# Kernel optimization log

Hardware: AMD Instinct MI355X
Metric: run time of the kernel (lower is better)

Reference implementation:

```python
import jax, jax.numpy as jnp
import numpy as np

EPS = 1e-5

def _conv3x3(x, w, b):
    # standard 3x3 conv, stride 1, padding 1, NCHW/OIHW
    y = jax.lax.conv_general_dilated(x, w, window_strides=(1, 1), padding=((1, 1), (1, 1)),
                                     dimension_numbers=('NCHW', 'OIHW', 'NCHW'))
    return y + b[None, :, None, None]

def _deform_sample(x, offset):
    # x: [B,C,H,W], offset: [B,2*9,H,W] (per kernel point: (dy,dx), torchvision layout)
    # returns bilinear-sampled im2col columns [B,C,9,H,W] with zero padding outside
    B, C, H, W = x.shape
    off = offset.reshape(B, 9, 2, H, W)
    off_y, off_x = off[:, :, 0], off[:, :, 1]                      # [B,9,H,W]
    k = jnp.arange(9)
    ky = (k // 3 - 1).astype(x.dtype)                               # kernel dy in {-1,0,1}
    kx = (k % 3 - 1).astype(x.dtype)                                # kernel dx in {-1,0,1}
    py = jnp.arange(H, dtype=x.dtype)[None, None, :, None] + ky[None, :, None, None] + off_y
    px = jnp.arange(W, dtype=x.dtype)[None, None, None, :] + kx[None, :, None, None] + off_x
    y0 = jnp.floor(py)
    x0 = jnp.floor(px)
    xf = x.reshape(B, C, H * W)
    acc = jnp.zeros((B, C, 9, H, W), x.dtype)
    for dy in (0.0, 1.0):
        for dx in (0.0, 1.0):
            iy = y0 + dy
            ix = x0 + dx
            wgt = (1.0 - jnp.abs(py - iy)) * (1.0 - jnp.abs(px - ix))
            valid = (iy >= 0) & (iy <= H - 1) & (ix >= 0) & (ix <= W - 1)
            wgt = jnp.where(valid, wgt, 0.0)
            idx = jnp.clip(iy, 0, H - 1).astype(jnp.int32) * W + jnp.clip(ix, 0, W - 1).astype(jnp.int32)
            g = jax.vmap(lambda xb, ib: jnp.take(xb, ib, axis=1))(xf, idx.reshape(B, -1))
            acc = acc + wgt[:, None] * g.reshape(B, C, 9, H, W)
    return acc

def setup_inputs() -> dict:
    key = jax.random.key(0)
    ks = jax.random.split(key, 9)
    B, C, O, H, W = 8, 64, 64, 160, 160
    x = jax.random.normal(ks[0], (B, C, H, W), jnp.float32)
    w_off = jax.random.normal(ks[1], (18, C, 3, 3), jnp.float32) * 0.01
    b_off = jax.random.normal(ks[2], (18,), jnp.float32) * 0.01
    w_dcn = jax.random.normal(ks[3], (O, C, 3, 3), jnp.float32) / np.sqrt(C * 9)
    b_dcn = jax.random.normal(ks[4], (O,), jnp.float32) * 0.01
    gamma = 1.0 + 0.1 * jax.random.normal(ks[5], (O,), jnp.float32)
    beta = 0.1 * jax.random.normal(ks[6], (O,), jnp.float32)
    run_mean = 0.1 * jax.random.normal(ks[7], (O,), jnp.float32)
    run_var = 0.5 + jax.random.uniform(ks[8], (O,), jnp.float32)
    return {"x": x, "w_off": w_off, "b_off": b_off, "w_dcn": w_dcn, "b_dcn": b_dcn,
            "gamma": gamma, "beta": beta, "run_mean": run_mean, "run_var": run_var}

def reference(x, w_off, b_off, w_dcn, b_dcn, gamma, beta, run_mean, run_var):
    offset = _conv3x3(x, w_off, b_off)                  # [B,18,H,W]
    cols = _deform_sample(x, offset)                    # [B,C,9,H,W]
    O = w_dcn.shape[0]
    z = jnp.einsum('bckhw,ock->bohw', cols, w_dcn.reshape(O, -1, 9)) + b_dcn[None, :, None, None]
    inv = gamma / jnp.sqrt(run_var + EPS)               # eval-mode BatchNorm
    y = z * inv[None, :, None, None] + (beta - run_mean * inv)[None, :, None, None]
    return jax.nn.relu(y)
```

## Files before the change

kernel.cpp:

```cpp
#include <hip/hip_runtime.h>

#define Hh 160
#define Ww 160
#define HW 25600
#define Bb 8
#define Cc 64
#define Oo 64
#define NPIX (Bb * HW)

#define TROWS 8
#define TCOLS 36
#define TPIX (TROWS * TCOLS)

typedef __bf16 bf16x8 __attribute__((ext_vector_type(8)));
typedef float  f32x4  __attribute__((ext_vector_type(4)));
typedef float  f32x2  __attribute__((ext_vector_type(2)));

__device__ inline unsigned rnd_bf(float a) {
    unsigned u = __float_as_uint(a);
    return (u + 0x7FFFu + ((u >> 16) & 1u)) >> 16;
}
__device__ inline unsigned cvtpk(float a, float b) {
    unsigned r;
    asm("v_cvt_pk_bf16_f32 %0, %1, %2" : "=v"(r) : "v"(a), "v"(b));
    return r;
}
__device__ inline f32x2 up2(unsigned u) {
    f32x2 r;
    r.x = __uint_as_float(u << 16);
    r.y = __uint_as_float(u & 0xffff0000u);
    return r;
}
__device__ inline unsigned blend4(unsigned u00, unsigned u01, unsigned u10, unsigned u11,
                                  float w00, float w01, float w10, float w11) {
    f32x2 r = up2(u00) * w00 + up2(u01) * w01 + up2(u10) * w10 + up2(u11) * w11;
    return cvtpk(r.x, r.y);
}
union UV { uint4 u; bf16x8 v; };
__device__ inline bf16x8 as_bf(uint4 u) { UV c; c.u = u; return c.v; }

__global__ __launch_bounds__(256) void prep_kernel(
    const float* __restrict__ w_dcn, const float* __restrict__ b_dcn,
    const float* __restrict__ w_off,
    const float* __restrict__ gamma, const float* __restrict__ beta,
    const float* __restrict__ run_mean, const float* __restrict__ run_var,
    unsigned short* __restrict__ wtbf, unsigned short* __restrict__ wofbf,
    float* __restrict__ scaleb)
{
    int i = blockIdx.x * 256 + threadIdx.x;
    if (i < 9 * 8 * 64 * 8) {
        int j = i & 7, l = (i >> 3) & 63, f = (i >> 9) & 7, k = i >> 12;
        int o  = ((f >> 1) << 4) | (l & 15);
        int cc = ((l >> 4) << 3) + ((f & 1) << 5) + j;
        wtbf[i] = (unsigned short)rnd_bf(w_dcn[(o * Cc + cc) * 9 + k]);
    }
    if (i < 9 * 4 * 64 * 8) {
        int j = i & 7, l = (i >> 3) & 63, f = (i >> 9) & 3, k = i >> 11;
        int o  = ((f >> 1) << 4) | (l & 15);
        int cc = ((l >> 4) << 3) + ((f & 1) << 5) + j;
        float v = (o < 18) ? w_off[(o * Cc + cc) * 9 + k] : 0.0f;
        wofbf[i] = (unsigned short)rnd_bf(v);
    }
    if (i < Oo) {
        float inv = gamma[i] * rsqrtf(run_var[i] + 1e-5f);
        scaleb[i]      = inv;
        scaleb[Oo + i] = b_dcn[i] * inv + (beta[i] - run_mean[i] * inv);
    }
}

#define TRD(PIX, LO, HI) do {                                                  \
    int _pp = (PIX);                                                           \
    int _s  = _pp & 7;                                                         \
    const char* _tb = (const char*)tile + _pp * 128;                           \
    LO = *(const uint4*)(_tb + ((quad ^ _s) << 4));                            \
    HI = *(const uint4*)(_tb + (((quad + 4) ^ _s) << 4));                      \
} while (0)

#define GATHF(CY, CX, A, H) do {                                               \
    const float* _sp = xbf + (size_t)(quad * 8) * HW + ((CY) * Ww + (CX));     \
    A = make_uint4(cvtpk(_sp[0],      _sp[HW]),                                \
                   cvtpk(_sp[2 * HW], _sp[3 * HW]),                            \
                   cvtpk(_sp[4 * HW], _sp[5 * HW]),                            \
                   cvtpk(_sp[6 * HW], _sp[7 * HW]));                           \
    const float* _hp = _sp + (size_t)32 * HW;                                  \
    H = make_uint4(cvtpk(_hp[0],      _hp[HW]),                                \
                   cvtpk(_hp[2 * HW], _hp[3 * HW]),                            \
                   cvtpk(_hp[4 * HW], _hp[5 * HW]),                            \
                   cvtpk(_hp[6 * HW], _hp[7 * HW]));                           \
} while (0)

__global__ __launch_bounds__(512, 6) void dcn_kernel(
    const float* __restrict__ x,
    const unsigned short* __restrict__ wtbf,
    const unsigned short* __restrict__ wofbf,
    const float* __restrict__ b_off,
    const float* __restrict__ scaleb,
    float* __restrict__ out)
{
    __shared__ __align__(16) unsigned short tile[TPIX * 64];

    const int t = threadIdx.x;
    const int lane = t & 63, wv = t >> 6;
    const int m = lane & 15, quad = lane >> 4;

    int blk = blockIdx.x;
    int b   = blk & 7;
    int nb  = blk >> 3;
    int h0  = (nb / 5) * 4;
    int w0  = (nb % 5) * 32;

    const int rloc  = wv >> 1;
    const int chalf = (wv & 1) * 16;
    const int h = h0 + rloc;
    const int w = w0 + chalf + m;
    const int pl_base = rloc * 32 + chalf;

    const float* xbf = x + (size_t)b * Cc * HW;

#pragma unroll
    for (int it = 0; it < 18; ++it) {
        int id  = t + it * 512;
        int col = id % 36;
        int rr  = id / 36;
        int r   = rr & 7;
        int c2  = rr >> 3;
        int yr = min(max(h0 - 2 + r, 0), Hh - 1);
        int xc = min(max(w0 - 2 + col, 0), Ww - 1);
        const float* sp = xbf + (size_t)(c2 * 2) * HW + (yr * Ww + xc);
        unsigned v = cvtpk(sp[0], sp[HW]);
        int pix = r * TCOLS + col;
        *(unsigned*)((char*)tile + pix * 128
                     + ((((c2 >> 2) ^ (pix & 7)) << 4) + ((c2 & 3) << 2))) = v;
    }
    __syncthreads();

    f32x4 oa0 = {0,0,0,0}, oa1 = {0,0,0,0};
#pragma unroll
    for (int k = 0; k < 9; ++k) {
        int hp = h + k / 3 - 1, wp = w + (k % 3) - 1;
        bool ok = (hp >= 0) & (hp < Hh) & (wp >= 0) & (wp < Ww);
        int r = min(max(hp, 0), Hh - 1) - h0 + 2;
        int c = min(max(wp, 0), Ww - 1) - w0 + 2;
        uint4 r0, r1;
        TRD(r * TCOLS + c, r0, r1);
        if (!ok) { r0 = make_uint4(0,0,0,0); r1 = make_uint4(0,0,0,0); }
        bf16x8 a0 = as_bf(r0), a1 = as_bf(r1);

        const unsigned short* wf = wofbf + (size_t)(k * 4) * 512 + lane * 8;
        bf16x8 b00 = *(const bf16x8*)(wf);
        bf16x8 b01 = *(const bf16x8*)(wf + 512);
        bf16x8 b10 = *(const bf16x8*)(wf + 1024);
        bf16x8 b11 = *(const bf16x8*)(wf + 1536);
        oa0 = __builtin_amdgcn_mfma_f32_16x16x32_bf16(b00, a0, oa0, 0, 0, 0);
        oa0 = __builtin_amdgcn_mfma_f32_16x16x32_bf16(b01, a1, oa0, 0, 0, 0);
        oa1 = __builtin_amdgcn_mfma_f32_16x16x32_bf16(b10, a0, oa1, 0, 0, 0);
        oa1 = __builtin_amdgcn_mfma_f32_16x16x32_bf16(b11, a1, oa1, 0, 0, 0);
    }

    float oy[9], ox[9];
#pragma unroll
    for (int k = 0; k < 9; ++k) {
        int cy = 2 * k, cx = 2 * k + 1;
        float vy = (cy < 16) ? __shfl(oa0[cy & 3], ((cy >> 2) << 4) + m, 64)
                             : __shfl(oa1[(cy - 16) & 3], (((cy - 16) >> 2) << 4) + m, 64);
        float vx = (cx < 16) ? __shfl(oa0[cx & 3], ((cx >> 2) << 4) + m, 64)
                             : __shfl(oa1[(cx - 16) & 3], (((cx - 16) >> 2) << 4) + m, 64);
        oy[k] = vy + b_off[cy];
        ox[k] = vx + b_off[cx];
    }

    f32x4 c0 = {0,0,0,0}, c1 = {0,0,0,0}, c2 = {0,0,0,0}, c3 = {0,0,0,0};
#pragma unroll
    for (int k = 0; k < 9; ++k) {
        float py = (float)(h + k / 3 - 1) + oy[k];
        float px = (float)(w + k % 3 - 1) + ox[k];
        float y0f = floorf(py), x0f = floorf(px);
        float fy = py - y0f, fx = px - x0f;
        int y0 = (int)y0f, x0i = (int)x0f;
        int y1 = y0 + 1, x1 = x0i + 1;
        bool vy0 = (y0 >= 0) & (y0 < Hh), vy1 = (y1 >= 0) & (y1 < Hh);
        bool vx0 = (x0i >= 0) & (x0i < Ww), vx1 = (x1 >= 0) & (x1 < Ww);
        float w00 = (vy0 & vx0) ? (1.0f - fy) * (1.0f - fx) : 0.0f;
        float w01 = (vy0 & vx1) ? (1.0f - fy) * fx : 0.0f;
        float w10 = (vy1 & vx0) ? fy * (1.0f - fx) : 0.0f;
        float w11 = (vy1 & vx1) ? fy * fx : 0.0f;
        int cy0 = min(max(y0, 0), Hh - 1), cy1 = min(max(y1, 0), Hh - 1);
        int cx0 = min(max(x0i, 0), Ww - 1), cx1 = min(max(x1, 0), Ww - 1);

        int r0 = cy0 - h0 + 2, r1 = cy1 - h0 + 2;
        int d0 = cx0 - w0 + 2, d1 = cx1 - w0 + 2;
        int inw = ((unsigned)r0 <= 7u) & ((unsigned)r1 <= 7u) &
                  ((unsigned)d0 <= 35u) & ((unsigned)d1 <= 35u);

        uint4 a00, h00, a01, h01, a10, h10, a11, h11;
        if (__all(inw)) {
            TRD(r0 * TCOLS + d0, a00, h00);
            TRD(r0 * TCOLS + d1, a01, h01);
            TRD(r1 * TCOLS + d0, a10, h10);
            TRD(r1 * TCOLS + d1, a11, h11);
        } else {
            GATHF(cy0, cx0, a00, h00);
            GATHF(cy0, cx1, a01, h01);
            GATHF(cy1, cx0, a10, h10);
            GATHF(cy1, cx1, a11, h11);
        }

        uint4 o0, o1;
        o0.x = blend4(a00.x, a01.x, a10.x, a11.x, w00, w01, w10, w11);
        o0.y = blend4(a00.y, a01.y, a10.y, a11.y, w00, w01, w10, w11);
        o0.z = blend4(a00.z, a01.z, a10.z, a11.z, w00, w01, w10, w11);
        o0.w = blend4(a00.w, a01.w, a10.w, a11.w, w00, w01, w10, w11);
        o1.x = blend4(h00.x, h01.x, h10.x, h11.x, w00, w01, w10, w11);
        o1.y = blend4(h00.y, h01.y, h10.y, h11.y, w00, w01, w10, w11);
        o1.z = blend4(h00.z, h01.z, h10.z, h11.z, w00, w01, w10, w11);
        o1.w = blend4(h00.w, h01.w, h10.w, h11.w, w00, w01, w10, w11);
        bf16x8 A0 = as_bf(o0), A1 = as_bf(o1);

        const unsigned short* wf = wtbf + (size_t)(k * 8) * 512 + lane * 8;
        bf16x8 B0, B1;
        B0 = *(const bf16x8*)(wf);
        B1 = *(const bf16x8*)(wf + 512);
        c0 = __builtin_amdgcn_mfma_f32_16x16x32_bf16(A0, B0, c0, 0, 0, 0);
        c0 = __builtin_amdgcn_mfma_f32_16x16x32_bf16(A1, B1, c0, 0, 0, 0);
        B0 = *(const bf16x8*)(wf + 1024);
        B1 = *(const bf16x8*)(wf + 1536);
        c1 = __builtin_amdgcn_mfma_f32_16x16x32_bf16(A0, B0, c1, 0, 0, 0);
        c1 = __builtin_amdgcn_mfma_f32_16x16x32_bf16(A1, B1, c1, 0, 0, 0);
        B0 = *(const bf16x8*)(wf + 2048);
        B1 = *(const bf16x8*)(wf + 2560);
        c2 = __builtin_amdgcn_mfma_f32_16x16x32_bf16(A0, B0, c2, 0, 0, 0);
        c2 = __builtin_amdgcn_mfma_f32_16x16x32_bf16(A1, B1, c2, 0, 0, 0);
        B0 = *(const bf16x8*)(wf + 3072);
        B1 = *(const bf16x8*)(wf + 3584);
        c3 = __builtin_amdgcn_mfma_f32_16x16x32_bf16(A0, B0, c3, 0, 0, 0);
        c3 = __builtin_amdgcn_mfma_f32_16x16x32_bf16(A1, B1, c3, 0, 0, 0);
    }

    __syncthreads();
    float* obuf = (float*)tile;
#pragma unroll
    for (int nt = 0; nt < 4; ++nt) {
        f32x4 a = (nt == 0) ? c0 : (nt == 1) ? c1 : (nt == 2) ? c2 : c3;
        int o = nt * 16 + m;
        float sc = scaleb[o];
        float bs = scaleb[Oo + o];
        f32x4 r;
        r[0] = fmaxf(a[0] * sc + bs, 0.0f);
        r[1] = fmaxf(a[1] * sc + bs, 0.0f);
        r[2] = fmaxf(a[2] * sc + bs, 0.0f);
        r[3] = fmaxf(a[3] * sc + bs, 0.0f);
        *(f32x4*)&obuf[o * 132 + pl_base + quad * 4] = r;
    }
    __syncthreads();
    {
        int o = t >> 3, c8 = t & 7;
        const float* src = obuf + o * 132 + c8 * 4;
        float* dst = out + ((size_t)b * Oo + o) * HW + h0 * Ww + w0 + c8 * 4;
#pragma unroll
        for (int j = 0; j < 4; ++j) {
            float4 v = *(const float4*)(src + j * 32);
            *(float4*)(dst + (size_t)j * Ww) = v;
        }
    }
}

extern "C" void kernel_launch(void* const* d_in, const int* in_sizes, int n_in,
                              void* d_out, int out_size, void* d_ws, size_t ws_size,
                              hipStream_t stream) {
    const float* x        = (const float*)d_in[0];
    const float* w_off    = (const float*)d_in[1];
    const float* b_off    = (const float*)d_in[2];
    const float* w_dcn    = (const float*)d_in[3];
    const float* b_dcn    = (const float*)d_in[4];
    const float* gamma    = (const float*)d_in[5];
    const float* beta     = (const float*)d_in[6];
    const float* run_mean = (const float*)d_in[7];
    const float* run_var  = (const float*)d_in[8];
    float* out = (float*)d_out;

    unsigned short* wtbf  = (unsigned short*)d_ws;
    unsigned short* wofbf = wtbf + 9 * 8 * 64 * 8;
    float* scaleb         = (float*)(wofbf + 9 * 4 * 64 * 8);

    prep_kernel<<<(9 * 8 * 64 * 8 + 255) / 256, 256, 0, stream>>>(
        w_dcn, b_dcn, w_off, gamma, beta, run_mean, run_var, wtbf, wofbf, scaleb);

    dcn_kernel<<<NPIX / 128, 512, 0, stream>>>(x, wtbf, wofbf, b_off, scaleb, out);
}
```

Baseline: 195.6 us.

## Software-pipeline deformable gathers with double-buffered registers across kernel points

```diff
diff --git a/kernel.cpp b/kernel.cpp
--- a/kernel.cpp
+++ b/kernel.cpp
@@ -89,7 +89,9 @@
                    cvtpk(_hp[6 * HW], _hp[7 * HW]));                           \
 } while (0)
 
-__global__ __launch_bounds__(512, 6) void dcn_kernel(
+struct GBuf { uint4 g[8]; float w[4]; };
+
+__global__ __launch_bounds__(512, 4) void dcn_kernel(
     const float* __restrict__ x,
     const unsigned short* __restrict__ wtbf,
     const unsigned short* __restrict__ wofbf,
@@ -157,84 +159,100 @@
         oa1 = __builtin_amdgcn_mfma_f32_16x16x32_bf16(b11, a1, oa1, 0, 0, 0);
     }
 
-    float oy[9], ox[9];
-#pragma unroll
-    for (int k = 0; k < 9; ++k) {
-        int cy = 2 * k, cx = 2 * k + 1;
-        float vy = (cy < 16) ? __shfl(oa0[cy & 3], ((cy >> 2) << 4) + m, 64)
-                             : __shfl(oa1[(cy - 16) & 3], (((cy - 16) >> 2) << 4) + m, 64);
-        float vx = (cx < 16) ? __shfl(oa0[cx & 3], ((cx >> 2) << 4) + m, 64)
-                             : __shfl(oa1[(cx - 16) & 3], (((cx - 16) >> 2) << 4) + m, 64);
-        oy[k] = vy + b_off[cy];
-        ox[k] = vx + b_off[cx];
-    }
-
     f32x4 c0 = {0,0,0,0}, c1 = {0,0,0,0}, c2 = {0,0,0,0}, c3 = {0,0,0,0};
-#pragma unroll
-    for (int k = 0; k < 9; ++k) {
-        float py = (float)(h + k / 3 - 1) + oy[k];
-        float px = (float)(w + k % 3 - 1) + ox[k];
-        float y0f = floorf(py), x0f = floorf(px);
-        float fy = py - y0f, fx = px - x0f;
-        int y0 = (int)y0f, x0i = (int)x0f;
-        int y1 = y0 + 1, x1 = x0i + 1;
-        bool vy0 = (y0 >= 0) & (y0 < Hh), vy1 = (y1 >= 0) & (y1 < Hh);
-        bool vx0 = (x0i >= 0) & (x0i < Ww), vx1 = (x1 >= 0) & (x1 < Ww);
-        float w00 = (vy0 & vx0) ? (1.0f - fy) * (1.0f - fx) : 0.0f;
-        float w01 = (vy0 & vx1) ? (1.0f - fy) * fx : 0.0f;
-        float w10 = (vy1 & vx0) ? fy * (1.0f - fx) : 0.0f;
-        float w11 = (vy1 & vx1) ? fy * fx : 0.0f;
-        int cy0 = min(max(y0, 0), Hh - 1), cy1 = min(max(y1, 0), Hh - 1);
-        int cx0 = min(max(x0i, 0), Ww - 1), cx1 = min(max(x1, 0), Ww - 1);
-
-        int r0 = cy0 - h0 + 2, r1 = cy1 - h0 + 2;
-        int d0 = cx0 - w0 + 2, d1 = cx1 - w0 + 2;
-        int inw = ((unsigned)r0 <= 7u) & ((unsigned)r1 <= 7u) &
-                  ((unsigned)d0 <= 35u) & ((unsigned)d1 <= 35u);
-
-        uint4 a00, h00, a01, h01, a10, h10, a11, h11;
-        if (__all(inw)) {
-            TRD(r0 * TCOLS + d0, a00, h00);
-            TRD(r0 * TCOLS + d1, a01, h01);
-            TRD(r1 * TCOLS + d0, a10, h10);
-            TRD(r1 * TCOLS + d1, a11, h11);
-        } else {
-            GATHF(cy0, cx0, a00, h00);
-            GATHF(cy0, cx1, a01, h01);
-            GATHF(cy1, cx0, a10, h10);
-            GATHF(cy1, cx1, a11, h11);
-        }
-
-        uint4 o0, o1;
-        o0.x = blend4(a00.x, a01.x, a10.x, a11.x, w00, w01, w10, w11);
-        o0.y = blend4(a00.y, a01.y, a10.y, a11.y, w00, w01, w10, w11);
-        o0.z = blend4(a00.z, a01.z, a10.z, a11.z, w00, w01, w10, w11);
-        o0.w = blend4(a00.w, a01.w, a10.w, a11.w, w00, w01, w10, w11);
-        o1.x = blend4(h00.x, h01.x, h10.x, h11.x, w00, w01, w10, w11);
-        o1.y = blend4(h00.y, h01.y, h10.y, h11.y, w00, w01, w10, w11);
-        o1.z = blend4(h00.z, h01.z, h10.z, h11.z, w00, w01, w10, w11);
-        o1.w = blend4(h00.w, h01.w, h10.w, h11.w, w00, w01, w10, w11);
-        bf16x8 A0 = as_bf(o0), A1 = as_bf(o1);
-
-        const unsigned short* wf = wtbf + (size_t)(k * 8) * 512 + lane * 8;
-        bf16x8 B0, B1;
-        B0 = *(const bf16x8*)(wf);
-        B1 = *(const bf16x8*)(wf + 512);
-        c0 = __builtin_amdgcn_mfma_f32_16x16x32_bf16(A0, B0, c0, 0, 0, 0);
-        c0 = __builtin_amdgcn_mfma_f32_16x16x32_bf16(A1, B1, c0, 0, 0, 0);
-        B0 = *(const bf16x8*)(wf + 1024);
-        B1 = *(const bf16x8*)(wf + 1536);
-        c1 = __builtin_amdgcn_mfma_f32_16x16x32_bf16(A0, B0, c1, 0, 0, 0);
-        c1 = __builtin_amdgcn_mfma_f32_16x16x32_bf16(A1, B1, c1, 0, 0, 0);
-        B0 = *(const bf16x8*)(wf + 2048);
-        B1 = *(const bf16x8*)(wf + 2560);
-        c2 = __builtin_amdgcn_mfma_f32_16x16x32_bf16(A0, B0, c2, 0, 0, 0);
-        c2 = __builtin_amdgcn_mfma_f32_16x16x32_bf16(A1, B1, c2, 0, 0, 0);
-        B0 = *(const bf16x8*)(wf + 3072);
-        B1 = *(const bf16x8*)(wf + 3584);
-        c3 = __builtin_amdgcn_mfma_f32_16x16x32_bf16(A0, B0, c3, 0, 0, 0);
-        c3 = __builtin_amdgcn_mfma_f32_16x16x32_bf16(A1, B1, c3, 0, 0, 0);
-    }
+
+#define OFFCH(C) ((C) < 16 ? __shfl(oa0[(C) & 3], (((C) >> 2) << 4) + m, 64)   \
+                           : __shfl(oa1[((C) - 16) & 3],                       \
+                                    ((((C) - 16) >> 2) << 4) + m, 64))
+
+#define ISSUE(K, X) do {                                                       \
+    float _oy = OFFCH(2 * (K))     + b_off[2 * (K)];                           \
+    float _ox = OFFCH(2 * (K) + 1) + b_off[2 * (K) + 1];                       \
+    float _py = (float)(h + (K) / 3 - 1) + _oy;                                \
+    float _px = (float)(w + (K) % 3 - 1) + _ox;                                \
+    float _y0f = floorf(_py), _x0f = floorf(_px);                              \
+    float _fy = _py - _y0f, _fx = _px - _x0f;                                  \
+    int _y0 = (int)_y0f, _x0 = (int)_x0f;                                      \
+    int _y1 = _y0 + 1, _x1 = _x0 + 1;                                          \
+    bool _vy0 = (_y0 >= 0) & (_y0 < Hh), _vy1 = (_y1 >= 0) & (_y1 < Hh);       \
+    bool _vx0 = (_x0 >= 0) & (_x0 < Ww), _vx1 = (_x1 >= 0) & (_x1 < Ww);       \
+    X.w[0] = (_vy0 & _vx0) ? (1.0f - _fy) * (1.0f - _fx) : 0.0f;               \
+    X.w[1] = (_vy0 & _vx1) ? (1.0f - _fy) * _fx : 0.0f;                        \
+    X.w[2] = (_vy1 & _vx0) ? _fy * (1.0f - _fx) : 0.0f;                        \
+    X.w[3] = (_vy1 & _vx1) ? _fy * _fx : 0.0f;                                 \
+    int _cy0 = min(max(_y0, 0), Hh - 1), _cy1 = min(max(_y1, 0), Hh - 1);      \
+    int _cx0 = min(max(_x0, 0), Ww - 1), _cx1 = min(max(_x1, 0), Ww - 1);      \
+    int _r0 = _cy0 - h0 + 2, _r1 = _cy1 - h0 + 2;                              \
+    int _d0 = _cx0 - w0 + 2, _d1 = _cx1 - w0 + 2;                              \
+    int _inw = ((unsigned)_r0 <= 7u) & ((unsigned)_r1 <= 7u) &                 \
+               ((unsigned)_d0 <= 35u) & ((unsigned)_d1 <= 35u);                \
+    if (__all(_inw)) {                                                         \
+        TRD(_r0 * TCOLS + _d0, X.g[0], X.g[1]);                                \
+        TRD(_r0 * TCOLS + _d1, X.g[2], X.g[3]);                                \
+        TRD(_r1 * TCOLS + _d0, X.g[4], X.g[5]);                                \
+        TRD(_r1 * TCOLS + _d1, X.g[6], X.g[7]);                                \
+    } else {                                                                   \
+        GATHF(_cy0, _cx0, X.g[0], X.g[1]);                                     \
+        GATHF(_cy0, _cx1, X.g[2], X.g[3]);                                     \
+        GATHF(_cy1, _cx0, X.g[4], X.g[5]);                                     \
+        GATHF(_cy1, _cx1, X.g[6], X.g[7]);                                     \
+    }                                                                          \
+} while (0)
+
+#define MATH(K, X) do {                                                        \
+    uint4 _o0, _o1;                                                            \
+    _o0.x = blend4(X.g[0].x, X.g[2].x, X.g[4].x, X.g[6].x,                     \
+                   X.w[0], X.w[1], X.w[2], X.w[3]);                            \
+    _o0.y = blend4(X.g[0].y, X.g[2].y, X.g[4].y, X.g[6].y,                     \
+                   X.w[0], X.w[1], X.w[2], X.w[3]);                            \
+    _o0.z = blend4(X.g[0].z, X.g[2].z, X.g[4].z, X.g[6].z,                     \
+                   X.w[0], X.w[1], X.w[2], X.w[3]);                            \
+    _o0.w = blend4(X.g[0].w, X.g[2].w, X.g[4].w, X.g[6].w,                     \
+                   X.w[0], X.w[1], X.w[2], X.w[3]);                            \
+    _o1.x = blend4(X.g[1].x, X.g[3].x, X.g[5].x, X.g[7].x,                     \
+                   X.w[0], X.w[1], X.w[2], X.w[3]);                            \
+    _o1.y = blend4(X.g[1].y, X.g[3].y, X.g[5].y, X.g[7].y,                     \
+                   X.w[0], X.w[1], X.w[2], X.w[3]);                            \
+    _o1.z = blend4(X.g[1].z, X.g[3].z, X.g[5].z, X.g[7].z,                     \
+                   X.w[0], X.w[1], X.w[2], X.w[3]);                            \
+    _o1.w = blend4(X.g[1].w, X.g[3].w, X.g[5].w, X.g[7].w,                     \
+                   X.w[0], X.w[1], X.w[2], X.w[3]);                            \
+    bf16x8 _A0 = as_bf(_o0), _A1 = as_bf(_o1);                                 \
+    const unsigned short* _wf = wtbf + (size_t)((K) * 8) * 512 + lane * 8;     \
+    bf16x8 _B0, _B1;                                                           \
+    _B0 = *(const bf16x8*)(_wf);                                               \
+    _B1 = *(const bf16x8*)(_wf + 512);                                         \
+    c0 = __builtin_amdgcn_mfma_f32_16x16x32_bf16(_A0, _B0, c0, 0, 0, 0);       \
+    c0 = __builtin_amdgcn_mfma_f32_16x16x32_bf16(_A1, _B1, c0, 0, 0, 0);       \
+    _B0 = *(const bf16x8*)(_wf + 1024);                                        \
+    _B1 = *(const bf16x8*)(_wf + 1536);                                        \
+    c1 = __builtin_amdgcn_mfma_f32_16x16x32_bf16(_A0, _B0, c1, 0, 0, 0);       \
+    c1 = __builtin_amdgcn_mfma_f32_16x16x32_bf16(_A1, _B1, c1, 0, 0, 0);       \
+    _B0 = *(const bf16x8*)(_wf + 2048);                                        \
+    _B1 = *(const bf16x8*)(_wf + 2560);                                        \
+    c2 = __builtin_amdgcn_mfma_f32_16x16x32_bf16(_A0, _B0, c2, 0, 0, 0);       \
+    c2 = __builtin_amdgcn_mfma_f32_16x16x32_bf16(_A1, _B1, c2, 0, 0, 0);       \
+    _B0 = *(const bf16x8*)(_wf + 3072);                                        \
+    _B1 = *(const bf16x8*)(_wf + 3584);                                        \
+    c3 = __builtin_amdgcn_mfma_f32_16x16x32_bf16(_A0, _B0, c3, 0, 0, 0);       \
+    c3 = __builtin_amdgcn_mfma_f32_16x16x32_bf16(_A1, _B1, c3, 0, 0, 0);       \
+} while (0)
+
+    GBuf Ga, Gb;
+    ISSUE(0, Ga);
+    ISSUE(1, Gb); MATH(0, Ga);
+    ISSUE(2, Ga); MATH(1, Gb);
+    ISSUE(3, Gb); MATH(2, Ga);
+    ISSUE(4, Ga); MATH(3, Gb);
+    ISSUE(5, Gb); MATH(4, Ga);
+    ISSUE(6, Ga); MATH(5, Gb);
+    ISSUE(7, Gb); MATH(6, Ga);
+    ISSUE(8, Ga); MATH(7, Gb);
+    MATH(8, Ga);
+
+#undef MATH
+#undef ISSUE
+#undef OFFCH
 
     __syncthreads();
     float* obuf = (float*)tile;
```

Result: faster. 189.4 us (-3.2%).
